# Kernel optimization log

Hardware: AMD Instinct MI355X
Metric: run time of the kernel (lower is better)

## Reference

```python
import jax, jax.numpy as jnp
import numpy as np

BN_EPS = 1e-5

def _l2norm(x, axis):
    return x / (1e-6 + jnp.linalg.norm(x, axis=axis, keepdims=True))

def setup_inputs() -> dict:
    key = jax.random.key(0)
    ks = jax.random.split(key, 4)
    c, k = 512, 64
    b, h, w = 16, 64, 64
    x = jax.random.normal(ks[0], (b, c, h, w), dtype=jnp.float32)
    conv1_w = jax.random.normal(ks[1], (c, c), dtype=jnp.float32) * np.sqrt(2.0 / c)
    conv1_b = jnp.zeros((c,), dtype=jnp.float32)
    mu = jax.random.normal(ks[2], (1, c, k), dtype=jnp.float32) * np.sqrt(2.0 / k)
    mu = _l2norm(mu, axis=1)
    conv2_w = jax.random.normal(ks[3], (c, c), dtype=jnp.float32) * np.sqrt(2.0 / c)
    bn_gamma = jnp.ones((c,), dtype=jnp.float32)
    bn_beta = jnp.zeros((c,), dtype=jnp.float32)
    bn_mean = jnp.zeros((c,), dtype=jnp.float32)
    bn_var = jnp.ones((c,), dtype=jnp.float32)
    return {"x": x, "conv1_w": conv1_w, "conv1_b": conv1_b, "mu": mu,
            "conv2_w": conv2_w, "bn_gamma": bn_gamma, "bn_beta": bn_beta,
            "bn_mean": bn_mean, "bn_var": bn_var}

STAGE_NUM = 3

def reference(x, conv1_w, conv1_b, mu, conv2_w, bn_gamma, bn_beta, bn_mean, bn_var):
    idn = x
    b, c, h, w = x.shape
    # conv1: 1x1 conv with bias
    xf = jnp.einsum('oc,bchw->bohw', conv1_w, x) + conv1_b[None, :, None, None]
    xf = xf.reshape(b, c, h * w)            # [b, c, n]
    mu_b = jnp.broadcast_to(mu, (b,) + mu.shape[1:])  # [b, c, k]

    # EM iterations (no-grad in original; here just the forward loop)
    def em_step(mu_b, _):
        z = jnp.einsum('bcn,bck->bnk', xf, mu_b)          # [b, n, k]
        z = jax.nn.softmax(z, axis=2)
        z_ = z / (1e-6 + z.sum(axis=1, keepdims=True))
        mu_new = _l2norm(jnp.einsum('bcn,bnk->bck', xf, z_), axis=1)
        return mu_new, z

    mu_b, zs = jax.lax.scan(em_step, mu_b, None, length=STAGE_NUM)
    z = zs[-1]                                            # last-stage responsibilities
    mu_b = jax.lax.stop_gradient(mu_b)
    z = jax.lax.stop_gradient(z)

    xr = jnp.einsum('bck,bnk->bcn', mu_b, z).reshape(b, c, h, w)
    xr = jax.nn.relu(xr)
    # conv2: 1x1 conv (no bias) + BatchNorm (inference mode)
    xr = jnp.einsum('oc,bchw->bohw', conv2_w, xr)
    inv = bn_gamma / jnp.sqrt(bn_var + BN_EPS)
    xr = xr * inv[None, :, None, None] + (bn_beta - bn_mean * inv)[None, :, None, None]
    return jax.nn.relu(xr + idn)
```

## Files before the change

kernel.cpp:

```cpp
#include <hip/hip_runtime.h>

typedef __bf16 bf16x8 __attribute__((ext_vector_type(8)));
typedef __bf16 bf16x4 __attribute__((ext_vector_type(4)));
typedef float f32x4 __attribute__((ext_vector_type(4)));

constexpr int CC = 512;
constexpr int KK = 64;
constexpr int NN = 4096;
constexpr int BB = 16;

constexpr size_t R1_OFF    = 0;
constexpr size_t R2_OFF    = 16777216;
constexpr size_t Z_OFF     = 33554432;
constexpr size_t ZT_OFF    = 35651584;
constexpr size_t MUACC_OFF = 37748736;
constexpr size_t ZSUM_OFF  = 38273024;
constexpr size_t MUBF_OFF  = 38274048;
constexpr size_t MUTBF_OFF = 38536192;
constexpr size_t W1BF_OFF  = 38798336;
constexpr size_t W2BF_OFF  = 38929408;

__global__ __launch_bounds__(256) void k_cvt2(const float* __restrict__ w1,
                                              const float* __restrict__ w2,
                                              __bf16* __restrict__ d1,
                                              __bf16* __restrict__ d2) {
    int blk = blockIdx.x;
    const float* src = (blk < 128) ? w1 : w2;
    __bf16* dst = (blk < 128) ? d1 : d2;
    int i = (blk & 127) * 256 + threadIdx.x;
    const float4* s4 = (const float4*)src;
    float4 a = s4[i * 2], b = s4[i * 2 + 1];
    bf16x8 o;
    o[0] = (__bf16)a.x; o[1] = (__bf16)a.y; o[2] = (__bf16)a.z; o[3] = (__bf16)a.w;
    o[4] = (__bf16)b.x; o[5] = (__bf16)b.y; o[6] = (__bf16)b.z; o[7] = (__bf16)b.w;
    *(bf16x8*)&dst[(size_t)i * 8] = o;
}

__global__ __launch_bounds__(256) void k_mu_bcast_bf(const float* __restrict__ mu_in,
                                                     __bf16* __restrict__ mu_bf,
                                                     __bf16* __restrict__ muT_bf) {
    int idx = blockIdx.x * 256 + threadIdx.x;
    if (idx < CC * KK) {
        int c = idx >> 6, k = idx & 63;
        __bf16 v = (__bf16)mu_in[idx];
        for (int b = 0; b < BB; ++b) {
            mu_bf[(size_t)b * CC * KK + idx] = v;
            muT_bf[((size_t)b * KK + k) * CC + c] = v;
        }
    }
}

__global__ __launch_bounds__(256) void k_xpose_cvt(const float* __restrict__ X,
                                                   __bf16* __restrict__ XT) {
    int n0 = blockIdx.x * 64, c0 = blockIdx.y * 64, b = blockIdx.z;
    __shared__ float T[64][65];
    int tid = threadIdx.x;
    const float* Xb = X + (size_t)b * CC * NN;
#pragma unroll
    for (int p = 0; p < 4; ++p) {
        int f4 = tid + p * 256;
        int row = f4 >> 4, col4 = (f4 & 15) * 4;
        float4 v = *(const float4*)&Xb[(size_t)(c0 + row) * NN + n0 + col4];
        T[row][col4 + 0] = v.x; T[row][col4 + 1] = v.y;
        T[row][col4 + 2] = v.z; T[row][col4 + 3] = v.w;
    }
    __syncthreads();
#pragma unroll
    for (int p = 0; p < 2; ++p) {
        int q = tid + p * 256;
        int nl = q >> 3, c8 = (q & 7) * 8;
        bf16x8 o;
#pragma unroll
        for (int j = 0; j < 8; ++j) o[j] = (__bf16)T[c8 + j][nl];
        *(bf16x8*)&XT[((size_t)b * NN + n0 + nl) * CC + c0 + c8] = o;
    }
}

__global__ __launch_bounds__(256) void k_conv1_mfma(
    const __bf16* __restrict__ XT, const __bf16* __restrict__ W1,
    const float* __restrict__ bias, __bf16* __restrict__ XFT,
    __bf16* __restrict__ XFC) {
    __shared__ __bf16 SM[17408];
    __shared__ float sbias[128];
    __bf16* As = SM;
    __bf16* Bs = SM + 8192;
    int tid = threadIdx.x;
    int lane = tid & 63, wave = tid >> 6;
    int wm = wave >> 1, wn = wave & 1;
    int o0 = blockIdx.x * 128, n0 = blockIdx.y * 128, b = blockIdx.z;
    const __bf16* Ab = XT + ((size_t)b * NN + n0) * CC;
    const __bf16* Bb = W1 + (size_t)o0 * CC;
    if (tid < 128) sbias[tid] = bias[o0 + tid];

    f32x4 acc[4][4];
#pragma unroll
    for (int i = 0; i < 4; ++i)
#pragma unroll
        for (int j = 0; j < 4; ++j) acc[i][j] = f32x4{0.f, 0.f, 0.f, 0.f};

    int r0 = tid >> 2, k0c = tid & 3;
    int r1 = (tid + 256) >> 2, k1c = tid & 3;
    int w0 = r0 * 32 + (k0c ^ ((r0 >> 1) & 3)) * 8;
    int w1 = r1 * 32 + (k1c ^ ((r1 >> 1) & 3)) * 8;

    bf16x8 va0, va1, vb0, vb1;
    va0 = *(const bf16x8*)(Ab + (size_t)r0 * CC + k0c * 8);
    va1 = *(const bf16x8*)(Ab + (size_t)r1 * CC + k1c * 8);
    vb0 = *(const bf16x8*)(Bb + (size_t)r0 * CC + k0c * 8);
    vb1 = *(const bf16x8*)(Bb + (size_t)r1 * CC + k1c * 8);
    *(bf16x8*)&As[w0] = va0; *(bf16x8*)&As[w1] = va1;
    *(bf16x8*)&Bs[w0] = vb0; *(bf16x8*)&Bs[w1] = vb1;
    __syncthreads();

    for (int kt = 0; kt < 16; ++kt) {
        int s = kt & 1;
        if (kt < 15) {
            const __bf16* Ak = Ab + (kt + 1) * 32;
            const __bf16* Bk = Bb + (kt + 1) * 32;
            va0 = *(const bf16x8*)(Ak + (size_t)r0 * CC + k0c * 8);
            va1 = *(const bf16x8*)(Ak + (size_t)r1 * CC + k1c * 8);
            vb0 = *(const bf16x8*)(Bk + (size_t)r0 * CC + k0c * 8);
            vb1 = *(const bf16x8*)(Bk + (size_t)r1 * CC + k1c * 8);
        }
        bf16x8 af[4], bg[4];
#pragma unroll
        for (int f = 0; f < 4; ++f) {
            int ra = wm * 64 + f * 16 + (lane & 15);
            af[f] = *(const bf16x8*)&As[s * 4096 + ra * 32 + (((lane >> 4) ^ ((ra >> 1) & 3))) * 8];
            int rb = wn * 64 + f * 16 + (lane & 15);
            bg[f] = *(const bf16x8*)&Bs[s * 4096 + rb * 32 + (((lane >> 4) ^ ((rb >> 1) & 3))) * 8];
        }
#pragma unroll
        for (int i = 0; i < 4; ++i)
#pragma unroll
            for (int j = 0; j < 4; ++j)
                acc[i][j] = __builtin_amdgcn_mfma_f32_16x16x32_bf16(af[i], bg[j], acc[i][j], 0, 0, 0);
        if (kt < 15) {
            *(bf16x8*)&As[(s ^ 1) * 4096 + w0] = va0; *(bf16x8*)&As[(s ^ 1) * 4096 + w1] = va1;
            *(bf16x8*)&Bs[(s ^ 1) * 4096 + w0] = vb0; *(bf16x8*)&Bs[(s ^ 1) * 4096 + w1] = vb1;
        }
        __syncthreads();
    }

    __bf16* TT = SM;
    int gq = lane >> 4, ln = lane & 15;
#pragma unroll
    for (int mf = 0; mf < 4; ++mf) {
#pragma unroll
        for (int nf = 0; nf < 4; ++nf) {
            int o_loc = wn * 64 + nf * 16 + ln;
            int n_loc4 = wm * 64 + mf * 16 + gq * 4;
            float bi = sbias[o_loc];
            bf16x4 oc;
#pragma unroll
            for (int r = 0; r < 4; ++r) oc[r] = (__bf16)(acc[mf][nf][r] + bi);
            *(bf16x4*)&XFC[((size_t)b * CC + o0 + o_loc) * NN + n0 + n_loc4] = oc;
#pragma unroll
            for (int r = 0; r < 4; ++r) TT[(n_loc4 + r) * 136 + o_loc] = oc[r];
        }
    }
    __syncthreads();
#pragma unroll
    for (int p = 0; p < 8; ++p) {
        int idx = tid + p * 256;
        int row = idx >> 4, ch = idx & 15;
        bf16x8 v = *(const bf16x8*)&TT[row * 136 + ch * 8];
        *(bf16x8*)&XFT[((size_t)b * NN + n0 + row) * CC + o0 + ch * 8] = v;
    }
}

__global__ __launch_bounds__(256) void k_conv2_mfma(
    const __bf16* __restrict__ W2, const __bf16* __restrict__ XRT,
    const float* __restrict__ gamma, const float* __restrict__ beta,
    const float* __restrict__ mean, const float* __restrict__ var,
    const float* __restrict__ Xres, float* __restrict__ Out) {
    __shared__ __bf16 As[2][128 * 32];
    __shared__ __bf16 Bs[2][128 * 32];
    __shared__ float sp0[128], sp1[128];
    int tid = threadIdx.x;
    int lane = tid & 63, wave = tid >> 6;
    int wm = wave >> 1, wn = wave & 1;
    int n0 = blockIdx.x * 128, m0 = blockIdx.y * 128, b = blockIdx.z;
    const __bf16* Ab = XRT + ((size_t)b * NN + n0) * CC;
    const __bf16* Bb = W2 + (size_t)m0 * CC;
    int gq = lane >> 4, ln = lane & 15;
    if (tid < 128) {
        float iv = gamma[m0 + tid] * rsqrtf(var[m0 + tid] + 1e-5f);
        sp0[tid] = iv;
        sp1[tid] = beta[m0 + tid] - mean[m0 + tid] * iv;
    }

    f32x4 xpre[4][4];
#pragma unroll
    for (int mf = 0; mf < 4; ++mf)
#pragma unroll
        for (int nf = 0; nf < 4; ++nf) {
            int o_loc = wn * 64 + nf * 16 + ln;
            int n_loc4 = wm * 64 + mf * 16 + gq * 4;
            xpre[mf][nf] = *(const f32x4*)&Xres[((size_t)b * CC + m0 + o_loc) * NN + n0 + n_loc4];
        }

    f32x4 acc[4][4];
#pragma unroll
    for (int i = 0; i < 4; ++i)
#pragma unroll
        for (int j = 0; j < 4; ++j) acc[i][j] = f32x4{0.f, 0.f, 0.f, 0.f};

    int r0 = tid >> 2, k0c = tid & 3;
    int r1 = (tid + 256) >> 2, k1c = tid & 3;
    int w0 = r0 * 32 + (k0c ^ ((r0 >> 1) & 3)) * 8;
    int w1 = r1 * 32 + (k1c ^ ((r1 >> 1) & 3)) * 8;

    bf16x8 va0, va1, vb0, vb1;
    va0 = *(const bf16x8*)(Ab + (size_t)r0 * CC + k0c * 8);
    va1 = *(const bf16x8*)(Ab + (size_t)r1 * CC + k1c * 8);
    vb0 = *(const bf16x8*)(Bb + (size_t)r0 * CC + k0c * 8);
    vb1 = *(const bf16x8*)(Bb + (size_t)r1 * CC + k1c * 8);
    *(bf16x8*)&As[0][w0] = va0; *(bf16x8*)&As[0][w1] = va1;
    *(bf16x8*)&Bs[0][w0] = vb0; *(bf16x8*)&Bs[0][w1] = vb1;
    __syncthreads();

    for (int kt = 0; kt < 16; ++kt) {
        int s = kt & 1;
        if (kt < 15) {
            const __bf16* Ak = Ab + (kt + 1) * 32;
            const __bf16* Bk = Bb + (kt + 1) * 32;
            va0 = *(const bf16x8*)(Ak + (size_t)r0 * CC + k0c * 8);
            va1 = *(const bf16x8*)(Ak + (size_t)r1 * CC + k1c * 8);
            vb0 = *(const bf16x8*)(Bk + (size_t)r0 * CC + k0c * 8);
            vb1 = *(const bf16x8*)(Bk + (size_t)r1 * CC + k1c * 8);
        }
        bf16x8 af[4], bg[4];
#pragma unroll
        for (int f = 0; f < 4; ++f) {
            int ra = wm * 64 + f * 16 + (lane & 15);
            af[f] = *(const bf16x8*)&As[s][ra * 32 + (((lane >> 4) ^ ((ra >> 1) & 3))) * 8];
            int rb = wn * 64 + f * 16 + (lane & 15);
            bg[f] = *(const bf16x8*)&Bs[s][rb * 32 + (((lane >> 4) ^ ((rb >> 1) & 3))) * 8];
        }
#pragma unroll
        for (int i = 0; i < 4; ++i)
#pragma unroll
            for (int j = 0; j < 4; ++j)
                acc[i][j] = __builtin_amdgcn_mfma_f32_16x16x32_bf16(af[i], bg[j], acc[i][j], 0, 0, 0);
        if (kt < 15) {
            *(bf16x8*)&As[s ^ 1][w0] = va0; *(bf16x8*)&As[s ^ 1][w1] = va1;
            *(bf16x8*)&Bs[s ^ 1][w0] = vb0; *(bf16x8*)&Bs[s ^ 1][w1] = vb1;
        }
        __syncthreads();
    }

#pragma unroll
    for (int mf = 0; mf < 4; ++mf) {
#pragma unroll
        for (int nf = 0; nf < 4; ++nf) {
            int o_loc = wn * 64 + nf * 16 + ln;
            int n_loc4 = wm * 64 + mf * 16 + gq * 4;
            size_t addr = ((size_t)b * CC + m0 + o_loc) * NN + n0 + n_loc4;
            float iv = sp0[o_loc], sh = sp1[o_loc];
            f32x4 xi = xpre[mf][nf];
            float4 v;
            v.x = fmaxf(acc[mf][nf][0] * iv + sh + xi[0], 0.f);
            v.y = fmaxf(acc[mf][nf][1] * iv + sh + xi[1], 0.f);
            v.z = fmaxf(acc[mf][nf][2] * iv + sh + xi[2], 0.f);
            v.w = fmaxf(acc[mf][nf][3] * iv + sh + xi[3], 0.f);
            *(float4*)&Out[addr] = v;
        }
    }
}

__global__ __launch_bounds__(256) void k_zsoftmax_mfma(
    const __bf16* __restrict__ XFT, const __bf16* __restrict__ MUT,
    __bf16* __restrict__ Z, __bf16* __restrict__ ZT, float* __restrict__ ZSUM,
    int write_z) {
    __shared__ __bf16 As[2][128 * 32];
    __shared__ __bf16 Bs[2][64 * 32];
    __shared__ __bf16 ZL[64][136];
    int tid = threadIdx.x;
    int lane = tid & 63, wave = tid >> 6;
    int n0 = blockIdx.x * 128, b = blockIdx.y;
    const __bf16* Ab = XFT + ((size_t)b * NN + n0) * CC;
    const __bf16* Bb = MUT + (size_t)b * KK * CC;

    f32x4 acc[2][4];
#pragma unroll
    for (int i = 0; i < 2; ++i)
#pragma unroll
        for (int j = 0; j < 4; ++j) acc[i][j] = f32x4{0.f, 0.f, 0.f, 0.f};

    int r0 = tid >> 2, k0c = tid & 3;
    int r1 = (tid + 256) >> 2, k1c = tid & 3;
    int w0 = r0 * 32 + (k0c ^ ((r0 >> 1) & 3)) * 8;
    int w1 = r1 * 32 + (k1c ^ ((r1 >> 1) & 3)) * 8;
    int rB = tid >> 2, kB = tid & 3;
    int wB = rB * 32 + (kB ^ ((rB >> 1) & 3)) * 8;

    bf16x8 va0, va1, vb0;
    va0 = *(const bf16x8*)(Ab + (size_t)r0 * CC + k0c * 8);
    va1 = *(const bf16x8*)(Ab + (size_t)r1 * CC + k1c * 8);
    vb0 = *(const bf16x8*)(Bb + (size_t)rB * CC + kB * 8);
    *(bf16x8*)&As[0][w0] = va0; *(bf16x8*)&As[0][w1] = va1;
    *(bf16x8*)&Bs[0][wB] = vb0;
    __syncthreads();

    for (int kt = 0; kt < 16; ++kt) {
        int s = kt & 1;
        if (kt < 15) {
            const __bf16* Ak = Ab + (kt + 1) * 32;
            const __bf16* Bk = Bb + (kt + 1) * 32;
            va0 = *(const bf16x8*)(Ak + (size_t)r0 * CC + k0c * 8);
            va1 = *(const bf16x8*)(Ak + (size_t)r1 * CC + k1c * 8);
            vb0 = *(const bf16x8*)(Bk + (size_t)rB * CC + kB * 8);
        }
        bf16x8 af[2], bg[4];
#pragma unroll
        for (int f = 0; f < 2; ++f) {
            int ra = wave * 32 + f * 16 + (lane & 15);
            af[f] = *(const bf16x8*)&As[s][ra * 32 + (((lane >> 4) ^ ((ra >> 1) & 3))) * 8];
        }
#pragma unroll
        for (int f = 0; f < 4; ++f) {
            int rb = f * 16 + (lane & 15);
            bg[f] = *(const bf16x8*)&Bs[s][rb * 32 + (((lane >> 4) ^ ((rb >> 1) & 3))) * 8];
        }
#pragma unroll
        for (int i = 0; i < 2; ++i)
#pragma unroll
            for (int j = 0; j < 4; ++j)
                acc[i][j] = __builtin_amdgcn_mfma_f32_16x16x32_bf16(af[i], bg[j], acc[i][j], 0, 0, 0);
        if (kt < 15) {
            *(bf16x8*)&As[s ^ 1][w0] = va0; *(bf16x8*)&As[s ^ 1][w1] = va1;
            *(bf16x8*)&Bs[s ^ 1][wB] = vb0;
        }
        __syncthreads();
    }

    int gq = lane >> 4, ln = lane & 15;
    float zp[4] = {0.f, 0.f, 0.f, 0.f};
#pragma unroll
    for (int mf = 0; mf < 2; ++mf) {
#pragma unroll
        for (int r = 0; r < 4; ++r) {
            float mx = fmaxf(fmaxf(acc[mf][0][r], acc[mf][1][r]),
                             fmaxf(acc[mf][2][r], acc[mf][3][r]));
            mx = fmaxf(mx, __shfl_xor(mx, 1));
            mx = fmaxf(mx, __shfl_xor(mx, 2));
            mx = fmaxf(mx, __shfl_xor(mx, 4));
            mx = fmaxf(mx, __shfl_xor(mx, 8));
            float e[4];
            float ssum = 0.f;
#pragma unroll
            for (int nf = 0; nf < 4; ++nf) { e[nf] = expf(acc[mf][nf][r] - mx); ssum += e[nf]; }
            ssum += __shfl_xor(ssum, 1);
            ssum += __shfl_xor(ssum, 2);
            ssum += __shfl_xor(ssum, 4);
            ssum += __shfl_xor(ssum, 8);
            float inv = 1.0f / ssum;
            int n_loc = wave * 32 + mf * 16 + gq * 4 + r;
#pragma unroll
            for (int nf = 0; nf < 4; ++nf) {
                float zv = e[nf] * inv;
                zp[nf] += zv;
                ZL[nf * 16 + ln][n_loc] = (__bf16)zv;
            }
        }
    }
#pragma unroll
    for (int nf = 0; nf < 4; ++nf) {
        float t = zp[nf];
        t += __shfl_xor(t, 16);
        t += __shfl_xor(t, 32);
        if (lane < 16) atomicAdd(&ZSUM[b * KK + nf * 16 + ln], t);
    }
    __syncthreads();
#pragma unroll
    for (int p = 0; p < 4; ++p) {
        int ci = tid + p * 256;
        int kr = ci >> 4, ch = (ci & 15) * 8;
        bf16x8 v = *(const bf16x8*)&ZL[kr][ch];
        *(bf16x8*)&ZT[((size_t)b * KK + kr) * NN + n0 + ch] = v;
    }
    if (write_z) {
#pragma unroll
        for (int p = 0; p < 4; ++p) {
            int idx = tid + p * 256;
            int row = idx >> 3, k8 = (idx & 7) * 8;
            bf16x8 o;
#pragma unroll
            for (int j = 0; j < 8; ++j) o[j] = ZL[k8 + j][row];
            *(bf16x8*)&Z[((size_t)b * NN + n0 + row) * KK + k8] = o;
        }
    }
}

__global__ __launch_bounds__(256) void k_muacc_mfma(
    const __bf16* __restrict__ XFC, const __bf16* __restrict__ ZT,
    float* __restrict__ MUACC) {
    __shared__ __bf16 As[2][128 * 32];
    __shared__ __bf16 Bs[2][64 * 32];
    int tid = threadIdx.x;
    int lane = tid & 63, wave = tid >> 6;
    int wm = wave >> 1, wn = wave & 1;
    int c0 = (blockIdx.x & 3) * 128, sp = blockIdx.x >> 2, b = blockIdx.y;
    size_t nbase = (size_t)sp * 512;
    const __bf16* Ab = XFC + ((size_t)b * CC + c0) * NN + nbase;
    const __bf16* Bb = ZT + (size_t)b * KK * NN + nbase;

    f32x4 acc[4][2];
#pragma unroll
    for (int i = 0; i < 4; ++i)
#pragma unroll
        for (int j = 0; j < 2; ++j) acc[i][j] = f32x4{0.f, 0.f, 0.f, 0.f};

    int r0 = tid >> 2, k0c = tid & 3;
    int r1 = (tid + 256) >> 2, k1c = tid & 3;
    int w0 = r0 * 32 + (k0c ^ ((r0 >> 1) & 3)) * 8;
    int w1 = r1 * 32 + (k1c ^ ((r1 >> 1) & 3)) * 8;
    int rB = tid >> 2, kB = tid & 3;
    int wB = rB * 32 + (kB ^ ((rB >> 1) & 3)) * 8;

    bf16x8 va0, va1, vb0;
    va0 = *(const bf16x8*)(Ab + (size_t)r0 * NN + k0c * 8);
    va1 = *(const bf16x8*)(Ab + (size_t)r1 * NN + k1c * 8);
    vb0 = *(const bf16x8*)(Bb + (size_t)rB * NN + kB * 8);
    *(bf16x8*)&As[0][w0] = va0; *(bf16x8*)&As[0][w1] = va1;
    *(bf16x8*)&Bs[0][wB] = vb0;
    __syncthreads();

    for (int kt = 0; kt < 16; ++kt) {
        int s = kt & 1;
        if (kt < 15) {
            const __bf16* Ak = Ab + (kt + 1) * 32;
            const __bf16* Bk = Bb + (kt + 1) * 32;
            va0 = *(const bf16x8*)(Ak + (size_t)r0 * NN + k0c * 8);
            va1 = *(const bf16x8*)(Ak + (size_t)r1 * NN + k1c * 8);
            vb0 = *(const bf16x8*)(Bk + (size_t)rB * NN + kB * 8);
        }
        bf16x8 af[4], bg[2];
#pragma unroll
        for (int f = 0; f < 4; ++f) {
            int ra = wm * 64 + f * 16 + (lane & 15);
            af[f] = *(const bf16x8*)&As[s][ra * 32 + (((lane >> 4) ^ ((ra >> 1) & 3))) * 8];
        }
#pragma unroll
        for (int f = 0; f < 2; ++f) {
            int rb = wn * 32 + f * 16 + (lane & 15);
            bg[f] = *(const bf16x8*)&Bs[s][rb * 32 + (((lane >> 4) ^ ((rb >> 1) & 3))) * 8];
        }
#pragma unroll
        for (int i = 0; i < 4; ++i)
#pragma unroll
            for (int j = 0; j < 2; ++j)
                acc[i][j] = __builtin_amdgcn_mfma_f32_16x16x32_bf16(af[i], bg[j], acc[i][j], 0, 0, 0);
        if (kt < 15) {
            *(bf16x8*)&As[s ^ 1][w0] = va0; *(bf16x8*)&As[s ^ 1][w1] = va1;
            *(bf16x8*)&Bs[s ^ 1][wB] = vb0;
        }
        __syncthreads();
    }

    int gq = lane >> 4, ln = lane & 15;
#pragma unroll
    for (int mf = 0; mf < 4; ++mf) {
#pragma unroll
        for (int r = 0; r < 4; ++r) {
            int row = wm * 64 + mf * 16 + gq * 4 + r;
#pragma unroll
            for (int nf = 0; nf < 2; ++nf) {
                int col = wn * 32 + nf * 16 + ln;
                atomicAdd(&MUACC[((size_t)b * CC + c0 + row) * KK + col], acc[mf][nf][r]);
            }
        }
    }
}

__global__ __launch_bounds__(64) void k_munorm_bf(
    float* __restrict__ MUACC, float* __restrict__ ZSUM,
    __bf16* __restrict__ mu_bf, __bf16* __restrict__ muT_bf) {
    int k = blockIdx.x;
    int b = blockIdx.y;
    int lane = threadIdx.x;
    float scale = 1.0f / (1e-6f + ZSUM[b * KK + k]);
    float v[8];
    float ss = 0.f;
#pragma unroll
    for (int i = 0; i < 8; ++i) {
        size_t a = (size_t)b * CC * KK + (size_t)(lane + i * 64) * KK + k;
        v[i] = MUACC[a] * scale;
        MUACC[a] = 0.f;
        ss += v[i] * v[i];
    }
    if (lane == 0) ZSUM[b * KK + k] = 0.f;
    for (int off = 32; off; off >>= 1) ss += __shfl_xor(ss, off);
    float nrm = 1.0f / (1e-6f + sqrtf(ss));
#pragma unroll
    for (int i = 0; i < 8; ++i) {
        int c = lane + i * 64;
        __bf16 o = (__bf16)(v[i] * nrm);
        mu_bf[((size_t)b * CC + c) * KK + k] = o;
        muT_bf[((size_t)b * KK + k) * CC + c] = o;
    }
}

__global__ __launch_bounds__(256) void k_xr_mfma(
    const __bf16* __restrict__ Zm, const __bf16* __restrict__ MUB,
    __bf16* __restrict__ XRT) {
    __shared__ __bf16 SM[17408];
    __bf16* As = SM;
    __bf16* Bs = SM + 8192;
    int tid = threadIdx.x;
    int lane = tid & 63, wave = tid >> 6;
    int wm = wave >> 1, wn = wave & 1;
    int n0 = blockIdx.x * 128, c0 = blockIdx.y * 128, b = blockIdx.z;
    const __bf16* Ab = Zm + ((size_t)b * NN + n0) * KK;
    const __bf16* Bb = MUB + ((size_t)b * CC + c0) * KK;
#pragma unroll
    for (int p = 0; p < 4; ++p) {
        int idx = tid + p * 256;
        int r = idx >> 3, ch = idx & 7;
        int woff = r * 64 + ((ch ^ (r & 7)) * 8);
        *(bf16x8*)&As[woff] = *(const bf16x8*)(Ab + (size_t)r * KK + ch * 8);
        *(bf16x8*)&Bs[woff] = *(const bf16x8*)(Bb + (size_t)r * KK + ch * 8);
    }
    __syncthreads();

    f32x4 acc[4][4];
#pragma unroll
    for (int i = 0; i < 4; ++i)
#pragma unroll
        for (int j = 0; j < 4; ++j) acc[i][j] = f32x4{0.f, 0.f, 0.f, 0.f};

    int gq = lane >> 4, ln = lane & 15;
#pragma unroll
    for (int ks = 0; ks < 2; ++ks) {
        bf16x8 af[4], bg[4];
#pragma unroll
        for (int f = 0; f < 4; ++f) {
            int ra = wm * 64 + f * 16 + ln;
            af[f] = *(const bf16x8*)&As[ra * 64 + (((ks * 4 + gq) ^ (ra & 7))) * 8];
            int rb = wn * 64 + f * 16 + ln;
            bg[f] = *(const bf16x8*)&Bs[rb * 64 + (((ks * 4 + gq) ^ (rb & 7))) * 8];
        }
#pragma unroll
        for (int i = 0; i < 4; ++i)
#pragma unroll
            for (int j = 0; j < 4; ++j)
                acc[i][j] = __builtin_amdgcn_mfma_f32_16x16x32_bf16(af[i], bg[j], acc[i][j], 0, 0, 0);
    }
    __syncthreads();

    __bf16* TT = SM;
#pragma unroll
    for (int mf = 0; mf < 4; ++mf) {
#pragma unroll
        for (int nf = 0; nf < 4; ++nf) {
            int c_loc = wn * 64 + nf * 16 + ln;
            int n_loc4 = wm * 64 + mf * 16 + gq * 4;
#pragma unroll
            for (int r = 0; r < 4; ++r)
                TT[(n_loc4 + r) * 136 + c_loc] = (__bf16)fmaxf(acc[mf][nf][r], 0.f);
        }
    }
    __syncthreads();
#pragma unroll
    for (int p = 0; p < 8; ++p) {
        int idx = tid + p * 256;
        int row = idx >> 4, ch = idx & 15;
        bf16x8 v = *(const bf16x8*)&TT[row * 136 + ch * 8];
        *(bf16x8*)&XRT[((size_t)b * NN + n0 + row) * CC + c0 + ch * 8] = v;
    }
}

extern "C" void kernel_launch(void* const* d_in, const int* in_sizes, int n_in,
                              void* d_out, int out_size, void* d_ws, size_t ws_size,
                              hipStream_t stream) {
    const float* x     = (const float*)d_in[0];
    const float* w1    = (const float*)d_in[1];
    const float* b1    = (const float*)d_in[2];
    const float* mu_in = (const float*)d_in[3];
    const float* w2    = (const float*)d_in[4];
    const float* gamma = (const float*)d_in[5];
    const float* beta  = (const float*)d_in[6];
    const float* mean  = (const float*)d_in[7];
    const float* var   = (const float*)d_in[8];
    float* out = (float*)d_out;
    float* ws  = (float*)d_ws;

    __bf16* xt    = (__bf16*)(ws + R1_OFF);
    __bf16* xft   = (__bf16*)(ws + R2_OFF);
    __bf16* xrt   = (__bf16*)(ws + R2_OFF);
    __bf16* xfc   = (__bf16*)d_out;
    __bf16* zbf   = (__bf16*)(ws + Z_OFF);
    __bf16* ztbf  = (__bf16*)(ws + ZT_OFF);
    float*  muacc = ws + MUACC_OFF;
    float*  zsum  = ws + ZSUM_OFF;
    __bf16* mu_bf = (__bf16*)(ws + MUBF_OFF);
    __bf16* muT_bf= (__bf16*)(ws + MUTBF_OFF);
    __bf16* w1bf  = (__bf16*)(ws + W1BF_OFF);
    __bf16* w2bf  = (__bf16*)(ws + W2BF_OFF);

    hipMemsetAsync(muacc, 0, (size_t)(BB * CC * KK + BB * KK) * sizeof(float), stream);
    hipLaunchKernelGGL(k_cvt2, dim3(256), dim3(256), 0, stream, w1, w2, w1bf, w2bf);
    hipLaunchKernelGGL(k_mu_bcast_bf, dim3(128), dim3(256), 0, stream, mu_in, mu_bf, muT_bf);
    hipLaunchKernelGGL(k_xpose_cvt, dim3(NN / 64, CC / 64, BB), dim3(256), 0, stream, x, xt);
    hipLaunchKernelGGL(k_conv1_mfma, dim3(CC / 128, NN / 128, BB), dim3(256), 0, stream,
                       xt, w1bf, b1, xft, xfc);
    for (int it = 0; it < 3; ++it) {
        hipLaunchKernelGGL(k_zsoftmax_mfma, dim3(NN / 128, BB), dim3(256), 0, stream,
                           xft, muT_bf, zbf, ztbf, zsum, (it == 2) ? 1 : 0);
        hipLaunchKernelGGL(k_muacc_mfma, dim3(32, BB), dim3(256), 0, stream, xfc, ztbf, muacc);
        hipLaunchKernelGGL(k_munorm_bf, dim3(KK, BB), dim3(64), 0, stream, muacc, zsum,
                           mu_bf, muT_bf);
    }
    hipLaunchKernelGGL(k_xr_mfma, dim3(NN / 128, CC / 128, BB), dim3(256), 0, stream,
                       zbf, mu_bf, xrt);
    hipLaunchKernelGGL(k_conv2_mfma, dim3(NN / 128, CC / 128, BB), dim3(256), 0, stream,
                       w2bf, xrt, gamma, beta, mean, var, x, out);
}
```

Measured before the change: 436.3 us.

## Deepen conv GEMM pipelines to triple-buffered LDS with two-stage register prefetch

Both conv1 and conv2 MFMA GEMM kernels move from a double-buffered LDS scheme with one register prefetch to a three-slot LDS ring fed by two alternating sets of prefetch registers. Global loads are issued two k-tiles ahead, so each load has more time to complete before its data is stored to LDS. The aim is to hide global-memory latency behind MFMA work. In exchange, LDS use per block grows by half and register pressure rises, which could lower occupancy.

```diff
diff --git a/kernel.cpp b/kernel.cpp
--- a/kernel.cpp
+++ b/kernel.cpp
@@ -80,10 +80,10 @@
     const __bf16* __restrict__ XT, const __bf16* __restrict__ W1,
     const float* __restrict__ bias, __bf16* __restrict__ XFT,
     __bf16* __restrict__ XFC) {
-    __shared__ __bf16 SM[17408];
+    __shared__ __bf16 SM[24576];
     __shared__ float sbias[128];
     __bf16* As = SM;
-    __bf16* Bs = SM + 8192;
+    __bf16* Bs = SM + 12288;
     int tid = threadIdx.x;
     int lane = tid & 63, wave = tid >> 6;
     int wm = wave >> 1, wn = wave & 1;
@@ -103,42 +103,59 @@
     int w0 = r0 * 32 + (k0c ^ ((r0 >> 1) & 3)) * 8;
     int w1 = r1 * 32 + (k1c ^ ((r1 >> 1) & 3)) * 8;
 
-    bf16x8 va0, va1, vb0, vb1;
-    va0 = *(const bf16x8*)(Ab + (size_t)r0 * CC + k0c * 8);
-    va1 = *(const bf16x8*)(Ab + (size_t)r1 * CC + k1c * 8);
-    vb0 = *(const bf16x8*)(Bb + (size_t)r0 * CC + k0c * 8);
-    vb1 = *(const bf16x8*)(Bb + (size_t)r1 * CC + k1c * 8);
-    *(bf16x8*)&As[w0] = va0; *(bf16x8*)&As[w1] = va1;
-    *(bf16x8*)&Bs[w0] = vb0; *(bf16x8*)&Bs[w1] = vb1;
-    __syncthreads();
-
-    for (int kt = 0; kt < 16; ++kt) {
-        int s = kt & 1;
-        if (kt < 15) {
-            const __bf16* Ak = Ab + (kt + 1) * 32;
-            const __bf16* Bk = Bb + (kt + 1) * 32;
-            va0 = *(const bf16x8*)(Ak + (size_t)r0 * CC + k0c * 8);
-            va1 = *(const bf16x8*)(Ak + (size_t)r1 * CC + k1c * 8);
-            vb0 = *(const bf16x8*)(Bk + (size_t)r0 * CC + k0c * 8);
-            vb1 = *(const bf16x8*)(Bk + (size_t)r1 * CC + k1c * 8);
-        }
+    bf16x8 sa0, sa1, sb0, sb1;
+    bf16x8 ta0, ta1, tb0, tb1;
+
+    auto LD0 = [&](int kt) {
+        const __bf16* Ak = Ab + kt * 32; const __bf16* Bk = Bb + kt * 32;
+        sa0 = *(const bf16x8*)(Ak + (size_t)r0 * CC + k0c * 8);
+        sa1 = *(const bf16x8*)(Ak + (size_t)r1 * CC + k1c * 8);
+        sb0 = *(const bf16x8*)(Bk + (size_t)r0 * CC + k0c * 8);
+        sb1 = *(const bf16x8*)(Bk + (size_t)r1 * CC + k1c * 8);
+    };
+    auto LD1 = [&](int kt) {
+        const __bf16* Ak = Ab + kt * 32; const __bf16* Bk = Bb + kt * 32;
+        ta0 = *(const bf16x8*)(Ak + (size_t)r0 * CC + k0c * 8);
+        ta1 = *(const bf16x8*)(Ak + (size_t)r1 * CC + k1c * 8);
+        tb0 = *(const bf16x8*)(Bk + (size_t)r0 * CC + k0c * 8);
+        tb1 = *(const bf16x8*)(Bk + (size_t)r1 * CC + k1c * 8);
+    };
+    auto ST0 = [&](int buf) {
+        *(bf16x8*)&As[buf * 4096 + w0] = sa0; *(bf16x8*)&As[buf * 4096 + w1] = sa1;
+        *(bf16x8*)&Bs[buf * 4096 + w0] = sb0; *(bf16x8*)&Bs[buf * 4096 + w1] = sb1;
+    };
+    auto ST1 = [&](int buf) {
+        *(bf16x8*)&As[buf * 4096 + w0] = ta0; *(bf16x8*)&As[buf * 4096 + w1] = ta1;
+        *(bf16x8*)&Bs[buf * 4096 + w0] = tb0; *(bf16x8*)&Bs[buf * 4096 + w1] = tb1;
+    };
+    auto MMA = [&](int buf) {
         bf16x8 af[4], bg[4];
 #pragma unroll
         for (int f = 0; f < 4; ++f) {
             int ra = wm * 64 + f * 16 + (lane & 15);
-            af[f] = *(const bf16x8*)&As[s * 4096 + ra * 32 + (((lane >> 4) ^ ((ra >> 1) & 3))) * 8];
+            af[f] = *(const bf16x8*)&As[buf * 4096 + ra * 32 + (((lane >> 4) ^ ((ra >> 1) & 3))) * 8];
             int rb = wn * 64 + f * 16 + (lane & 15);
-            bg[f] = *(const bf16x8*)&Bs[s * 4096 + rb * 32 + (((lane >> 4) ^ ((rb >> 1) & 3))) * 8];
+            bg[f] = *(const bf16x8*)&Bs[buf * 4096 + rb * 32 + (((lane >> 4) ^ ((rb >> 1) & 3))) * 8];
         }
 #pragma unroll
         for (int i = 0; i < 4; ++i)
 #pragma unroll
             for (int j = 0; j < 4; ++j)
                 acc[i][j] = __builtin_amdgcn_mfma_f32_16x16x32_bf16(af[i], bg[j], acc[i][j], 0, 0, 0);
-        if (kt < 15) {
-            *(bf16x8*)&As[(s ^ 1) * 4096 + w0] = va0; *(bf16x8*)&As[(s ^ 1) * 4096 + w1] = va1;
-            *(bf16x8*)&Bs[(s ^ 1) * 4096 + w0] = vb0; *(bf16x8*)&Bs[(s ^ 1) * 4096 + w1] = vb1;
-        }
+    };
+
+    LD0(0); ST0(0);
+    LD1(1);
+    __syncthreads();
+
+    for (int kt = 0; kt < 16; kt += 2) {
+        if (kt + 2 < 16) LD0(kt + 2);
+        MMA(kt % 3);
+        ST1((kt + 1) % 3);
+        __syncthreads();
+        if (kt + 3 < 16) LD1(kt + 3);
+        MMA((kt + 1) % 3);
+        if (kt + 2 < 16) ST0((kt + 2) % 3);
         __syncthreads();
     }
 
@@ -174,8 +191,8 @@
     const float* __restrict__ gamma, const float* __restrict__ beta,
     const float* __restrict__ mean, const float* __restrict__ var,
     const float* __restrict__ Xres, float* __restrict__ Out) {
-    __shared__ __bf16 As[2][128 * 32];
-    __shared__ __bf16 Bs[2][128 * 32];
+    __shared__ __bf16 As[3][4096];
+    __shared__ __bf16 Bs[3][4096];
     __shared__ float sp0[128], sp1[128];
     int tid = threadIdx.x;
     int lane = tid & 63, wave = tid >> 6;
@@ -190,6 +207,60 @@
         sp1[tid] = beta[m0 + tid] - mean[m0 + tid] * iv;
     }
 
+    f32x4 acc[4][4];
+#pragma unroll
+    for (int i = 0; i < 4; ++i)
+#pragma unroll
+        for (int j = 0; j < 4; ++j) acc[i][j] = f32x4{0.f, 0.f, 0.f, 0.f};
+
+    int r0 = tid >> 2, k0c = tid & 3;
+    int r1 = (tid + 256) >> 2, k1c = tid & 3;
+    int w0 = r0 * 32 + (k0c ^ ((r0 >> 1) & 3)) * 8;
+    int w1 = r1 * 32 + (k1c ^ ((r1 >> 1) & 3)) * 8;
+
+    bf16x8 sa0, sa1, sb0, sb1;
+    bf16x8 ta0, ta1, tb0, tb1;
+
+    auto LD0 = [&](int kt) {
+        const __bf16* Ak = Ab + kt * 32; const __bf16* Bk = Bb + kt * 32;
+        sa0 = *(const bf16x8*)(Ak + (size_t)r0 * CC + k0c * 8);
+        sa1 = *(const bf16x8*)(Ak + (size_t)r1 * CC + k1c * 8);
+        sb0 = *(const bf16x8*)(Bk + (size_t)r0 * CC + k0c * 8);
+        sb1 = *(const bf16x8*)(Bk + (size_t)r1 * CC + k1c * 8);
+    };
+    auto LD1 = [&](int kt) {
+        const __bf16* Ak = Ab + kt * 32; const __bf16* Bk = Bb + kt * 32;
+        ta0 = *(const bf16x8*)(Ak + (size_t)r0 * CC + k0c * 8);
+        ta1 = *(const bf16x8*)(Ak + (size_t)r1 * CC + k1c * 8);
+        tb0 = *(const bf16x8*)(Bk + (size_t)r0 * CC + k0c * 8);
+        tb1 = *(const bf16x8*)(Bk + (size_t)r1 * CC + k1c * 8);
+    };
+    auto ST0 = [&](int buf) {
+        *(bf16x8*)&As[buf][w0] = sa0; *(bf16x8*)&As[buf][w1] = sa1;
+        *(bf16x8*)&Bs[buf][w0] = sb0; *(bf16x8*)&Bs[buf][w1] = sb1;
+    };
+    auto ST1 = [&](int buf) {
+        *(bf16x8*)&As[buf][w0] = ta0; *(bf16x8*)&As[buf][w1] = ta1;
+        *(bf16x8*)&Bs[buf][w0] = tb0; *(bf16x8*)&Bs[buf][w1] = tb1;
+    };
+    auto MMA = [&](int buf) {
+        bf16x8 af[4], bg[4];
+#pragma unroll
+        for (int f = 0; f < 4; ++f) {
+            int ra = wm * 64 + f * 16 + (lane & 15);
+            af[f] = *(const bf16x8*)&As[buf][ra * 32 + (((lane >> 4) ^ ((ra >> 1) & 3))) * 8];
+            int rb = wn * 64 + f * 16 + (lane & 15);
+            bg[f] = *(const bf16x8*)&Bs[buf][rb * 32 + (((lane >> 4) ^ ((rb >> 1) & 3))) * 8];
+        }
+#pragma unroll
+        for (int i = 0; i < 4; ++i)
+#pragma unroll
+            for (int j = 0; j < 4; ++j)
+                acc[i][j] = __builtin_amdgcn_mfma_f32_16x16x32_bf16(af[i], bg[j], acc[i][j], 0, 0, 0);
+    };
+
+    LD0(0); ST0(0);
+    LD1(1);
     f32x4 xpre[4][4];
 #pragma unroll
     for (int mf = 0; mf < 4; ++mf)
@@ -199,54 +270,16 @@
             int n_loc4 = wm * 64 + mf * 16 + gq * 4;
             xpre[mf][nf] = *(const f32x4*)&Xres[((size_t)b * CC + m0 + o_loc) * NN + n0 + n_loc4];
         }
-
-    f32x4 acc[4][4];
-#pragma unroll
-    for (int i = 0; i < 4; ++i)
-#pragma unroll
-        for (int j = 0; j < 4; ++j) acc[i][j] = f32x4{0.f, 0.f, 0.f, 0.f};
-
-    int r0 = tid >> 2, k0c = tid & 3;
-    int r1 = (tid + 256) >> 2, k1c = tid & 3;
-    int w0 = r0 * 32 + (k0c ^ ((r0 >> 1) & 3)) * 8;
-    int w1 = r1 * 32 + (k1c ^ ((r1 >> 1) & 3)) * 8;
-
-    bf16x8 va0, va1, vb0, vb1;
-    va0 = *(const bf16x8*)(Ab + (size_t)r0 * CC + k0c * 8);
-    va1 = *(const bf16x8*)(Ab + (size_t)r1 * CC + k1c * 8);
-    vb0 = *(const bf16x8*)(Bb + (size_t)r0 * CC + k0c * 8);
-    vb1 = *(const bf16x8*)(Bb + (size_t)r1 * CC + k1c * 8);
-    *(bf16x8*)&As[0][w0] = va0; *(bf16x8*)&As[0][w1] = va1;
-    *(bf16x8*)&Bs[0][w0] = vb0; *(bf16x8*)&Bs[0][w1] = vb1;
-    __syncthreads();
-
-    for (int kt = 0; kt < 16; ++kt) {
-        int s = kt & 1;
-        if (kt < 15) {
-            const __bf16* Ak = Ab + (kt + 1) * 32;
-            const __bf16* Bk = Bb + (kt + 1) * 32;
-            va0 = *(const bf16x8*)(Ak + (size_t)r0 * CC + k0c * 8);
-            va1 = *(const bf16x8*)(Ak + (size_t)r1 * CC + k1c * 8);
-            vb0 = *(const bf16x8*)(Bk + (size_t)r0 * CC + k0c * 8);
-            vb1 = *(const bf16x8*)(Bk + (size_t)r1 * CC + k1c * 8);
-        }
-        bf16x8 af[4], bg[4];
-#pragma unroll
-        for (int f = 0; f < 4; ++f) {
-            int ra = wm * 64 + f * 16 + (lane & 15);
-            af[f] = *(const bf16x8*)&As[s][ra * 32 + (((lane >> 4) ^ ((ra >> 1) & 3))) * 8];
-            int rb = wn * 64 + f * 16 + (lane & 15);
-            bg[f] = *(const bf16x8*)&Bs[s][rb * 32 + (((lane >> 4) ^ ((rb >> 1) & 3))) * 8];
-        }
-#pragma unroll
-        for (int i = 0; i < 4; ++i)
-#pragma unroll
-            for (int j = 0; j < 4; ++j)
-                acc[i][j] = __builtin_amdgcn_mfma_f32_16x16x32_bf16(af[i], bg[j], acc[i][j], 0, 0, 0);
-        if (kt < 15) {
-            *(bf16x8*)&As[s ^ 1][w0] = va0; *(bf16x8*)&As[s ^ 1][w1] = va1;
-            *(bf16x8*)&Bs[s ^ 1][w0] = vb0; *(bf16x8*)&Bs[s ^ 1][w1] = vb1;
-        }
+    __syncthreads();
+
+    for (int kt = 0; kt < 16; kt += 2) {
+        if (kt + 2 < 16) LD0(kt + 2);
+        MMA(kt % 3);
+        ST1((kt + 1) % 3);
+        __syncthreads();
+        if (kt + 3 < 16) LD1(kt + 3);
+        MMA((kt + 1) % 3);
+        if (kt + 2 < 16) ST0((kt + 2) % 3);
         __syncthreads();
     }
 
```

New measurement: 429.7 us, median of 3. Within noise of the previous version (-1.5%).

## Deepen conv GEMM K-tile to 64 with two-stage register prefetch

Applied to the files above, without the earlier changes.

Both 1x1-conv MFMA GEMM kernels switch from 32-wide K tiles over 16 iterations to 64-wide K tiles over 8 iterations. They also use a new 8-way XOR LDS swizzle and a deeper pipeline that prefetches global tiles two steps ahead while storing the previous prefetch into the alternate LDS buffer. The aim is to halve the number of barriers per GEMM and hide global load latency better. LDS use rises to 64 KB per block and more prefetch registers are needed, which may lower occupancy.

```diff
diff --git a/kernel.cpp b/kernel.cpp
--- a/kernel.cpp
+++ b/kernel.cpp
@@ -80,13 +80,13 @@
     const __bf16* __restrict__ XT, const __bf16* __restrict__ W1,
     const float* __restrict__ bias, __bf16* __restrict__ XFT,
     __bf16* __restrict__ XFC) {
-    __shared__ __bf16 SM[17408];
+    __shared__ __bf16 As[2][8192];
+    __shared__ __bf16 Bs[2][8192];
     __shared__ float sbias[128];
-    __bf16* As = SM;
-    __bf16* Bs = SM + 8192;
     int tid = threadIdx.x;
     int lane = tid & 63, wave = tid >> 6;
     int wm = wave >> 1, wn = wave & 1;
+    int gq = lane >> 4, ln = lane & 15;
     int o0 = blockIdx.x * 128, n0 = blockIdx.y * 128, b = blockIdx.z;
     const __bf16* Ab = XT + ((size_t)b * NN + n0) * CC;
     const __bf16* Bb = W1 + (size_t)o0 * CC;
@@ -98,52 +98,56 @@
 #pragma unroll
         for (int j = 0; j < 4; ++j) acc[i][j] = f32x4{0.f, 0.f, 0.f, 0.f};
 
-    int r0 = tid >> 2, k0c = tid & 3;
-    int r1 = (tid + 256) >> 2, k1c = tid & 3;
-    int w0 = r0 * 32 + (k0c ^ ((r0 >> 1) & 3)) * 8;
-    int w1 = r1 * 32 + (k1c ^ ((r1 >> 1) & 3)) * 8;
-
-    bf16x8 va0, va1, vb0, vb1;
-    va0 = *(const bf16x8*)(Ab + (size_t)r0 * CC + k0c * 8);
-    va1 = *(const bf16x8*)(Ab + (size_t)r1 * CC + k1c * 8);
-    vb0 = *(const bf16x8*)(Bb + (size_t)r0 * CC + k0c * 8);
-    vb1 = *(const bf16x8*)(Bb + (size_t)r1 * CC + k1c * 8);
-    *(bf16x8*)&As[w0] = va0; *(bf16x8*)&As[w1] = va1;
-    *(bf16x8*)&Bs[w0] = vb0; *(bf16x8*)&Bs[w1] = vb1;
-    __syncthreads();
-
-    for (int kt = 0; kt < 16; ++kt) {
-        int s = kt & 1;
-        if (kt < 15) {
-            const __bf16* Ak = Ab + (kt + 1) * 32;
-            const __bf16* Bk = Bb + (kt + 1) * 32;
-            va0 = *(const bf16x8*)(Ak + (size_t)r0 * CC + k0c * 8);
-            va1 = *(const bf16x8*)(Ak + (size_t)r1 * CC + k1c * 8);
-            vb0 = *(const bf16x8*)(Bk + (size_t)r0 * CC + k0c * 8);
-            vb1 = *(const bf16x8*)(Bk + (size_t)r1 * CC + k1c * 8);
-        }
-        bf16x8 af[4], bg[4];
-#pragma unroll
-        for (int f = 0; f < 4; ++f) {
-            int ra = wm * 64 + f * 16 + (lane & 15);
-            af[f] = *(const bf16x8*)&As[s * 4096 + ra * 32 + (((lane >> 4) ^ ((ra >> 1) & 3))) * 8];
-            int rb = wn * 64 + f * 16 + (lane & 15);
-            bg[f] = *(const bf16x8*)&Bs[s * 4096 + rb * 32 + (((lane >> 4) ^ ((rb >> 1) & 3))) * 8];
-        }
-#pragma unroll
-        for (int i = 0; i < 4; ++i)
-#pragma unroll
-            for (int j = 0; j < 4; ++j)
-                acc[i][j] = __builtin_amdgcn_mfma_f32_16x16x32_bf16(af[i], bg[j], acc[i][j], 0, 0, 0);
-        if (kt < 15) {
-            *(bf16x8*)&As[(s ^ 1) * 4096 + w0] = va0; *(bf16x8*)&As[(s ^ 1) * 4096 + w1] = va1;
-            *(bf16x8*)&Bs[(s ^ 1) * 4096 + w0] = vb0; *(bf16x8*)&Bs[(s ^ 1) * 4096 + w1] = vb1;
-        }
+    bf16x8 va[4], vb[4];
+    auto LD = [&](int kt) {
+#pragma unroll
+        for (int p = 0; p < 4; ++p) {
+            int q = tid + p * 256;
+            int r = q >> 3, cx = q & 7;
+            va[p] = *(const bf16x8*)(Ab + (size_t)r * CC + kt * 64 + cx * 8);
+            vb[p] = *(const bf16x8*)(Bb + (size_t)r * CC + kt * 64 + cx * 8);
+        }
+    };
+    auto ST = [&](int buf) {
+#pragma unroll
+        for (int p = 0; p < 4; ++p) {
+            int q = tid + p * 256;
+            int r = q >> 3, cx = q & 7;
+            int w = r * 64 + ((cx ^ (r & 7)) * 8);
+            *(bf16x8*)&As[buf][w] = va[p];
+            *(bf16x8*)&Bs[buf][w] = vb[p];
+        }
+    };
+    auto MMA = [&](int buf) {
+#pragma unroll
+        for (int ks = 0; ks < 2; ++ks) {
+            bf16x8 af[4], bg[4];
+#pragma unroll
+            for (int f = 0; f < 4; ++f) {
+                int ra = wm * 64 + f * 16 + ln;
+                af[f] = *(const bf16x8*)&As[buf][ra * 64 + (((ks * 4 + gq) ^ (ra & 7))) * 8];
+                int rb = wn * 64 + f * 16 + ln;
+                bg[f] = *(const bf16x8*)&Bs[buf][rb * 64 + (((ks * 4 + gq) ^ (rb & 7))) * 8];
+            }
+#pragma unroll
+            for (int i = 0; i < 4; ++i)
+#pragma unroll
+                for (int j = 0; j < 4; ++j)
+                    acc[i][j] = __builtin_amdgcn_mfma_f32_16x16x32_bf16(af[i], bg[j], acc[i][j], 0, 0, 0);
+        }
+    };
+
+    LD(0); ST(0);
+    LD(1);
+    __syncthreads();
+    for (int kt = 0; kt < 8; ++kt) {
+        if (kt + 1 < 8) ST((kt + 1) & 1);
+        if (kt + 2 < 8) LD(kt + 2);
+        MMA(kt & 1);
         __syncthreads();
     }
 
-    __bf16* TT = SM;
-    int gq = lane >> 4, ln = lane & 15;
+    __bf16* TT = &As[0][0];
 #pragma unroll
     for (int mf = 0; mf < 4; ++mf) {
 #pragma unroll
@@ -174,22 +178,69 @@
     const float* __restrict__ gamma, const float* __restrict__ beta,
     const float* __restrict__ mean, const float* __restrict__ var,
     const float* __restrict__ Xres, float* __restrict__ Out) {
-    __shared__ __bf16 As[2][128 * 32];
-    __shared__ __bf16 Bs[2][128 * 32];
+    __shared__ __bf16 As[2][8192];
+    __shared__ __bf16 Bs[2][8192];
     __shared__ float sp0[128], sp1[128];
     int tid = threadIdx.x;
     int lane = tid & 63, wave = tid >> 6;
     int wm = wave >> 1, wn = wave & 1;
+    int gq = lane >> 4, ln = lane & 15;
     int n0 = blockIdx.x * 128, m0 = blockIdx.y * 128, b = blockIdx.z;
     const __bf16* Ab = XRT + ((size_t)b * NN + n0) * CC;
     const __bf16* Bb = W2 + (size_t)m0 * CC;
-    int gq = lane >> 4, ln = lane & 15;
     if (tid < 128) {
         float iv = gamma[m0 + tid] * rsqrtf(var[m0 + tid] + 1e-5f);
         sp0[tid] = iv;
         sp1[tid] = beta[m0 + tid] - mean[m0 + tid] * iv;
     }
 
+    f32x4 acc[4][4];
+#pragma unroll
+    for (int i = 0; i < 4; ++i)
+#pragma unroll
+        for (int j = 0; j < 4; ++j) acc[i][j] = f32x4{0.f, 0.f, 0.f, 0.f};
+
+    bf16x8 va[4], vb[4];
+    auto LD = [&](int kt) {
+#pragma unroll
+        for (int p = 0; p < 4; ++p) {
+            int q = tid + p * 256;
+            int r = q >> 3, cx = q & 7;
+            va[p] = *(const bf16x8*)(Ab + (size_t)r * CC + kt * 64 + cx * 8);
+            vb[p] = *(const bf16x8*)(Bb + (size_t)r * CC + kt * 64 + cx * 8);
+        }
+    };
+    auto ST = [&](int buf) {
+#pragma unroll
+        for (int p = 0; p < 4; ++p) {
+            int q = tid + p * 256;
+            int r = q >> 3, cx = q & 7;
+            int w = r * 64 + ((cx ^ (r & 7)) * 8);
+            *(bf16x8*)&As[buf][w] = va[p];
+            *(bf16x8*)&Bs[buf][w] = vb[p];
+        }
+    };
+    auto MMA = [&](int buf) {
+#pragma unroll
+        for (int ks = 0; ks < 2; ++ks) {
+            bf16x8 af[4], bg[4];
+#pragma unroll
+            for (int f = 0; f < 4; ++f) {
+                int ra = wm * 64 + f * 16 + ln;
+                af[f] = *(const bf16x8*)&As[buf][ra * 64 + (((ks * 4 + gq) ^ (ra & 7))) * 8];
+                int rb = wn * 64 + f * 16 + ln;
+                bg[f] = *(const bf16x8*)&Bs[buf][rb * 64 + (((ks * 4 + gq) ^ (rb & 7))) * 8];
+            }
+#pragma unroll
+            for (int i = 0; i < 4; ++i)
+#pragma unroll
+                for (int j = 0; j < 4; ++j)
+                    acc[i][j] = __builtin_amdgcn_mfma_f32_16x16x32_bf16(af[i], bg[j], acc[i][j], 0, 0, 0);
+        }
+    };
+
+    LD(0); ST(0);
+    LD(1);
     f32x4 xpre[4][4];
 #pragma unroll
     for (int mf = 0; mf < 4; ++mf)
@@ -199,54 +250,11 @@
             int n_loc4 = wm * 64 + mf * 16 + gq * 4;
             xpre[mf][nf] = *(const f32x4*)&Xres[((size_t)b * CC + m0 + o_loc) * NN + n0 + n_loc4];
         }
-
-    f32x4 acc[4][4];
-#pragma unroll
-    for (int i = 0; i < 4; ++i)
-#pragma unroll
-        for (int j = 0; j < 4; ++j) acc[i][j] = f32x4{0.f, 0.f, 0.f, 0.f};
-
-    int r0 = tid >> 2, k0c = tid & 3;
-    int r1 = (tid + 256) >> 2, k1c = tid & 3;
-    int w0 = r0 * 32 + (k0c ^ ((r0 >> 1) & 3)) * 8;
-    int w1 = r1 * 32 + (k1c ^ ((r1 >> 1) & 3)) * 8;
-
-    bf16x8 va0, va1, vb0, vb1;
-    va0 = *(const bf16x8*)(Ab + (size_t)r0 * CC + k0c * 8);
-    va1 = *(const bf16x8*)(Ab + (size_t)r1 * CC + k1c * 8);
-    vb0 = *(const bf16x8*)(Bb + (size_t)r0 * CC + k0c * 8);
-    vb1 = *(const bf16x8*)(Bb + (size_t)r1 * CC + k1c * 8);
-    *(bf16x8*)&As[0][w0] = va0; *(bf16x8*)&As[0][w1] = va1;
-    *(bf16x8*)&Bs[0][w0] = vb0; *(bf16x8*)&Bs[0][w1] = vb1;
-    __syncthreads();
-
-    for (int kt = 0; kt < 16; ++kt) {
-        int s = kt & 1;
-        if (kt < 15) {
-            const __bf16* Ak = Ab + (kt + 1) * 32;
-            const __bf16* Bk = Bb + (kt + 1) * 32;
-            va0 = *(const bf16x8*)(Ak + (size_t)r0 * CC + k0c * 8);
-            va1 = *(const bf16x8*)(Ak + (size_t)r1 * CC + k1c * 8);
-            vb0 = *(const bf16x8*)(Bk + (size_t)r0 * CC + k0c * 8);
-            vb1 = *(const bf16x8*)(Bk + (size_t)r1 * CC + k1c * 8);
-        }
-        bf16x8 af[4], bg[4];
-#pragma unroll
-        for (int f = 0; f < 4; ++f) {
-            int ra = wm * 64 + f * 16 + (lane & 15);
-            af[f] = *(const bf16x8*)&As[s][ra * 32 + (((lane >> 4) ^ ((ra >> 1) & 3))) * 8];
-            int rb = wn * 64 + f * 16 + (lane & 15);
-            bg[f] = *(const bf16x8*)&Bs[s][rb * 32 + (((lane >> 4) ^ ((rb >> 1) & 3))) * 8];
-        }
-#pragma unroll
-        for (int i = 0; i < 4; ++i)
-#pragma unroll
-            for (int j = 0; j < 4; ++j)
-                acc[i][j] = __builtin_amdgcn_mfma_f32_16x16x32_bf16(af[i], bg[j], acc[i][j], 0, 0, 0);
-        if (kt < 15) {
-            *(bf16x8*)&As[s ^ 1][w0] = va0; *(bf16x8*)&As[s ^ 1][w1] = va1;
-            *(bf16x8*)&Bs[s ^ 1][w0] = vb0; *(bf16x8*)&Bs[s ^ 1][w1] = vb1;
-        }
+    __syncthreads();
+    for (int kt = 0; kt < 8; ++kt) {
+        if (kt + 1 < 8) ST((kt + 1) & 1);
+        if (kt + 2 < 8) LD(kt + 2);
+        MMA(kt & 1);
         __syncthreads();
     }
 
```

Result: no change. 432.5 us (-0.9%).
